# Kernel optimization log

Measured on AMD Instinct MI355X. Metric: run time of the kernel, lower is better.

## Reference

```python
import jax, jax.numpy as jnp
import numpy as np

B, C, HZ, SX = 512, 112, 8, 16
P = HZ * HZ   # num_kernel = 64 template pixels
OC = 256
EPS = 1e-5

def _conv(x, w, pad, groups=1):
    return jax.lax.conv_general_dilated(
        x, w, (1, 1), [(pad, pad), (pad, pad)],
        feature_group_count=groups,
        dimension_numbers=('NCHW', 'OIHW', 'NCHW'))

def _bn(x, g, b, m, v):
    # eval-mode BatchNorm2d with running stats
    scale = (g / jnp.sqrt(v + EPS))[None, :, None, None]
    return (x - m[None, :, None, None]) * scale + b[None, :, None, None]

def setup_inputs() -> dict:
    key = jax.random.key(0)
    ks = jax.random.split(key, 16)
    n = lambda i, shape, s=0.05: jax.random.normal(ks[i], shape, dtype=jnp.float32) * s
    return dict(
        search=jax.random.normal(ks[0], (B, C, SX, SX), dtype=jnp.float32),
        kernel=jax.random.normal(ks[1], (B, C, HZ, HZ), dtype=jnp.float32),
        ca_w1=n(2, (P, P)), ca_b1=jnp.zeros((P,), jnp.float32),
        ca_w2=n(3, (P, P)), ca_b2=jnp.zeros((P,), jnp.float32),
        cls_dw=n(4, (P, 1, 3, 3)), cls_pw=n(5, (OC, P)),
        cls_bn_g=jnp.ones((OC,), jnp.float32), cls_bn_b=jnp.zeros((OC,), jnp.float32),
        cls_bn_m=n(6, (OC,)), cls_bn_v=jax.random.uniform(ks[7], (OC,), jnp.float32, 0.5, 1.5),
        cls_pred_w=n(8, (1, OC, 3, 3)), cls_pred_b=jnp.zeros((1,), jnp.float32),
        box_dw=n(9, (P, 1, 3, 3)), box_pw=n(10, (OC, P)),
        box_bn_g=jnp.ones((OC,), jnp.float32), box_bn_b=jnp.zeros((OC,), jnp.float32),
        box_bn_m=n(11, (OC,)), box_bn_v=jax.random.uniform(ks[12], (OC,), jnp.float32, 0.5, 1.5),
        box_pred_w=n(13, (4, OC, 3, 3)), box_pred_b=jnp.zeros((4,), jnp.float32),
        adjust=0.1 * jnp.ones((1,), jnp.float32),
        bias_p=jnp.ones((1, 4, 1, 1), jnp.float32),
    )

def reference(search, kernel, ca_w1, ca_b1, ca_w2, ca_b2,
              cls_dw, cls_pw, cls_bn_g, cls_bn_b, cls_bn_m, cls_bn_v,
              cls_pred_w, cls_pred_b,
              box_dw, box_pw, box_bn_g, box_bn_b, box_bn_m, box_bn_v,
              box_pred_w, box_pred_b, adjust, bias_p):
    b, c, h, w = search.shape
    # pixel-wise correlation (batched form of the per-sample F.conv2d loop):
    # corr[b,p,i,j] = sum_c kernel[b,c].flatten()[p] * search[b,c,i,j]
    z = kernel.reshape(b, c, -1)                       # [B, C, P]
    corr = jnp.einsum('bcp,bcij->bpij', z, search)      # [B, P, H, W]
    # channel attention (CAModule, reduction=1)
    s = corr.mean(axis=(2, 3))                          # [B, P]
    a = jax.nn.sigmoid(jax.nn.relu(s @ ca_w1.T + ca_b1) @ ca_w2.T + ca_b2)
    corr = corr * a[:, :, None, None]
    # cls tower: depthwise 3x3 -> pointwise -> BN -> ReLU
    cfeat = jnp.einsum('oc,bchw->bohw', cls_pw, _conv(corr, cls_dw, 1, groups=P))
    cfeat = jax.nn.relu(_bn(cfeat, cls_bn_g, cls_bn_b, cls_bn_m, cls_bn_v))
    cls = 0.1 * (_conv(cfeat, cls_pred_w, 1) + cls_pred_b[None, :, None, None])
    # bbox tower
    rfeat = jnp.einsum('oc,bchw->bohw', box_pw, _conv(corr, box_dw, 1, groups=P))
    rfeat = jax.nn.relu(_bn(rfeat, box_bn_g, box_bn_b, box_bn_m, box_bn_v))
    pred = _conv(rfeat, box_pred_w, 1) + box_pred_b[None, :, None, None]
    x = jnp.exp(adjust[0] * pred + bias_p)
    return (x, cls)
```

## Files before the change

### kernel.cpp

```cpp
#include <hip/hip_runtime.h>
#include <hip/hip_bf16.h>


typedef __attribute__((ext_vector_type(8))) short  bf16x8;
typedef __attribute__((ext_vector_type(4))) float  f32x4;

union U8 { bf16x8 v; uint4 q; unsigned short u[8]; };

__device__ __forceinline__ float bf2f(unsigned short h){
  union { unsigned int u; float f; } c; c.u = ((unsigned int)h) << 16; return c.f;
}
__device__ __forceinline__ unsigned short f2bf(float f){
  return __bfloat16_as_ushort(__float2bfloat16(f));
}
__device__ __forceinline__ unsigned int f2bf2(float lo, float hi){
  return (unsigned int)f2bf(lo) | ((unsigned int)f2bf(hi) << 16);
}

__device__ __forceinline__ int swz(int row, int pix){
  return row*256 + (((pix>>3) ^ (row&31))<<3) + (pix&7);
}
__device__ __forceinline__ int zt_off(int p, int c){
  return (p<<8) + ((((c>>3) ^ (p&15)) & 15)<<4) + ((c&7)<<1);
}
__device__ __forceinline__ int sT_off(int pix, int c){
  return (pix<<7) + ((((c>>3) ^ (pix&7) ^ ((pix>>3)&7)) & 7)<<4) + ((c&7)<<1);
}
__device__ __forceinline__ int dT_off(int pix, int p){
  return (pix<<7) + (((((p>>3) ^ pix) & 7)) << 4) + ((p & 7) << 1);
}
__device__ __forceinline__ int fT_off(int pix, int ocl){
  return (pix<<6) + ((((ocl>>3) ^ pix ^ (pix>>2)) & 3) << 4) + ((ocl & 7) << 1);
}
__device__ __forceinline__ int pA_off(int ocl, int p){
  return (ocl<<7) + (((((p>>3) ^ ocl) & 7)) << 4) + ((p & 7) << 1);
}

__device__ __forceinline__ void stage_pw(int tid, int oc0,
                                         const float* __restrict__ pw,
                                         unsigned char* __restrict__ dst){
  const int ocl = tid >> 4, p0 = (tid & 15) << 2;
  const float4 f0 = *(const float4*)&pw[(oc0 + ocl)*64 + p0];
  uint2 w; w.x = f2bf2(f0.x, f0.y); w.y = f2bf2(f0.z, f0.w);
  *(uint2*)(dst + pA_off(ocl, p0)) = w;
}

template<int NOUT>
__device__ __forceinline__ void stage_wA(int tid, int oc0,
                                         const float* __restrict__ pdw,
                                         unsigned char* __restrict__ dst){
  #pragma unroll
  for (int i=0;i<(NOUT*288+511)/512;++i){
    const int idx = i*512 + tid;
    if (idx < NOUT*288){
      const int o   = idx / 288;
      const int rem = idx - o*288;
      const int tau = rem >> 5, ocl = rem & 31;
      *(unsigned short*)(dst + (idx<<1)) =
          f2bf(pdw[(o*256 + oc0 + ocl)*9 + tau]);
    }
  }
}

template<int NOUT, bool DBUF>
__device__ __forceinline__ void run_tower(
    int tid, float ap,
    const float* __restrict__ dw,  const float* __restrict__ pw,
    const float* __restrict__ bng, const float* __restrict__ bnb,
    const float* __restrict__ bnm, const float* __restrict__ bnv,
    const float* __restrict__ pdw, const float* __restrict__ pdb,
    float* __restrict__ outp, float adj, const float* __restrict__ biasp,
    unsigned char* smem)
{
  const int lane = tid & 63, wave = tid >> 6;
  const int l15 = lane & 15, lg = lane >> 4;
  unsigned short* sA16 = (unsigned short*)smem;

  {
    const int p = lane;
    unsigned char* dT = smem + 32768;
    float wd[9];
    #pragma unroll
    for (int k=0;k<9;++k) wd[k] = dw[p*9+k] * ap;
    #pragma unroll
    for (int io=0;io<2;++io){
      const int ir = wave*2 + io;
      float ot[16];
      #pragma unroll
      for (int j=0;j<16;++j) ot[j] = 0.f;
      #pragma unroll
      for (int dr=0;dr<3;++dr){
        const int r = ir-1+dr;
        if (r >= 0 && r < 16){
          unsigned short tr[16];
          *(uint4*)&tr[0] = *(uint4*)&sA16[swz(p, r*16)];
          *(uint4*)&tr[8] = *(uint4*)&sA16[swz(p, r*16 + 8)];
          float rr[16];
          #pragma unroll
          for (int j=0;j<16;++j) rr[j] = bf2f(tr[j]);
          const float w0 = wd[dr*3+0], w1 = wd[dr*3+1], w2 = wd[dr*3+2];
          #pragma unroll
          for (int j=0;j<16;++j){
            float s = w1*rr[j];
            if (j > 0)  s = fmaf(w0, rr[j-1], s);
            if (j < 15) s = fmaf(w2, rr[j+1], s);
            ot[j] += s;
          }
        }
      }
      #pragma unroll
      for (int j=0;j<16;++j)
        *(unsigned short*)(dT + dT_off(ir*16+j, p)) = f2bf(ot[j]);
    }
  }
  __syncthreads();

  U8 bfr[2][2];
  #pragma unroll
  for (int nt=0;nt<2;++nt)
    #pragma unroll
    for (int ks=0;ks<2;++ks)
      bfr[nt][ks].q = *(const uint4*)(smem + 32768 +
          dT_off(wave*32 + nt*16 + l15, ks*32 + lg*8));
  __syncthreads();

  float* scl = (float*)(smem + 61952);
  float* bia = (float*)(smem + 62976);
  if (tid < 256){
    const float s = bng[tid] * rsqrtf(bnv[tid] + 1e-5f);
    scl[tid] = s;
    bia[tid] = bnb[tid] - bnm[tid]*s;
  }

  f32x4 accp[2];
  accp[0] = f32x4{0.f,0.f,0.f,0.f};
  accp[1] = f32x4{0.f,0.f,0.f,0.f};

  auto pw_chunk = [&](unsigned char* pAb, unsigned char* featb, int oc0){
    #pragma unroll
    for (int mt=0;mt<2;++mt){
      U8 af0, af1;
      af0.q = *(const uint4*)(pAb + pA_off(mt*16 + l15, lg*8));
      af1.q = *(const uint4*)(pAb + pA_off(mt*16 + l15, 32 + lg*8));
      f32x4 accw[2];
      accw[0] = f32x4{0.f,0.f,0.f,0.f};
      accw[1] = f32x4{0.f,0.f,0.f,0.f};
      #pragma unroll
      for (int nt=0;nt<2;++nt){
        accw[nt] = __builtin_amdgcn_mfma_f32_16x16x32_bf16(
            af0.v, bfr[nt][0].v, accw[nt], 0, 0, 0);
        accw[nt] = __builtin_amdgcn_mfma_f32_16x16x32_bf16(
            af1.v, bfr[nt][1].v, accw[nt], 0, 0, 0);
      }
      #pragma unroll
      for (int r=0;r<4;++r){
        const int ocl = mt*16 + lg*4 + r;
        const float sc = scl[oc0+ocl], bi = bia[oc0+ocl];
        #pragma unroll
        for (int nt=0;nt<2;++nt){
          const int pix = wave*32 + nt*16 + l15;
          const float v = fmaxf(fmaf(accw[nt][r], sc, bi), 0.f);
          *(unsigned short*)(featb + fT_off(pix, ocl)) = f2bf(v);
        }
      }
    }
  };

  auto pred_chunk = [&](unsigned char* featb, unsigned char* wAb){
    #pragma unroll
    for (int dr=0;dr<3;++dr){
      #pragma unroll
      for (int dc=0;dc<3;++dc){
        const int tau = dr*3 + dc;
        U8 a;
        const int mr = (NOUT == 4) ? (l15 & 3) : 0;
        a.q = *(const uint4*)(wAb + ((mr*288 + tau*32 + lg*8) << 1));
        if (l15 >= NOUT) a.q = make_uint4(0u,0u,0u,0u);
        #pragma unroll
        for (int nt=0;nt<2;++nt){
          const int rp = wave*2 + nt + dr - 1;
          if (rp >= 0 && rp <= 15){
            const int cp = l15 + dc - 1;
            const int cc = cp < 0 ? 0 : (cp > 15 ? 15 : cp);
            U8 bf;
            bf.q = *(const uint4*)(featb + fT_off(rp*16 + cc, lg*8));
            if (cp != cc) bf.q = make_uint4(0u,0u,0u,0u);
            accp[nt] = __builtin_amdgcn_mfma_f32_16x16x32_bf16(
                a.v, bf.v, accp[nt], 0, 0, 0);
          }
        }
      }
    }
  };

  if constexpr (!DBUF){
    stage_pw(tid, 0, pw, smem + 49152);
    stage_wA<NOUT>(tid, 0, pdw, smem + 57344);
    for (int ch=0; ch<8; ++ch){
      const int buf = ch & 1, oc0 = ch*32;
      __syncthreads();
      pw_chunk(smem + 49152 + buf*4096, smem + 32768, oc0);
      __syncthreads();
      if (ch < 7){
        stage_pw(tid, oc0 + 32, pw, smem + 49152 + (buf^1)*4096);
        stage_wA<NOUT>(tid, oc0 + 32, pdw, smem + 57344 + (buf^1)*2304);
      }
      pred_chunk(smem + 32768, smem + 57344 + buf*2304);
    }
    __syncthreads();
  } else {
    stage_pw(tid, 0,  pw, smem + 49152);
    stage_pw(tid, 32, pw, smem + 53248);
    stage_wA<NOUT>(tid, 0, pdw, smem + 57344);
    __syncthreads();
    pw_chunk(smem + 49152, smem + 0, 0);
    __syncthreads();
    for (int i=0; i<8; ++i){
      const int s = i & 1;
      if (i < 6) stage_pw(tid, (i+2)*32, pw, smem + 49152 + s*4096);
      if (i < 7) stage_wA<NOUT>(tid, (i+1)*32, pdw,
                                smem + 57344 + ((i+1)&1)*(NOUT*576));
      if (i < 7) pw_chunk(smem + 49152 + ((i+1)&1)*4096,
                          smem + ((i+1)&1)*16384, (i+1)*32);
      pred_chunk(smem + s*16384, smem + 57344 + s*(NOUT*576));
      __syncthreads();
    }
  }

  if (lane < 16){
    #pragma unroll
    for (int nt=0;nt<2;++nt){
      const int rt = wave*2 + nt;
      if constexpr (NOUT == 1){
        outp[rt*16 + lane] = 0.1f*(accp[nt][0] + pdb[0]);
      } else {
        #pragma unroll
        for (int o=0;o<4;++o)
          outp[o*256 + rt*16 + lane] =
              expf(fmaf(adj, accp[nt][o] + pdb[o], biasp[o]));
      }
    }
  }
}

__global__ __launch_bounds__(512, 4) void fused_head(
  const float* __restrict__ search, const float* __restrict__ kern,
  const float* __restrict__ ca_w1, const float* __restrict__ ca_b1,
  const float* __restrict__ ca_w2, const float* __restrict__ ca_b2,
  const float* __restrict__ cls_dw, const float* __restrict__ cls_pw,
  const float* __restrict__ cls_bn_g, const float* __restrict__ cls_bn_b,
  const float* __restrict__ cls_bn_m, const float* __restrict__ cls_bn_v,
  const float* __restrict__ cls_pred_w, const float* __restrict__ cls_pred_b,
  const float* __restrict__ box_dw, const float* __restrict__ box_pw,
  const float* __restrict__ box_bn_g, const float* __restrict__ box_bn_b,
  const float* __restrict__ box_bn_m, const float* __restrict__ box_bn_v,
  const float* __restrict__ box_pred_w, const float* __restrict__ box_pred_b,
  const float* __restrict__ adjust, const float* __restrict__ bias_p,
  float* __restrict__ out)
{
  __shared__ __align__(16) unsigned char smem[65536];
  const int b   = blockIdx.x;
  const int tid = threadIdx.x;
  const int lane = tid & 63, wave = tid >> 6;
  const int l15 = lane & 15, lg = lane >> 4;

  unsigned char* zb = smem;
  {
    const float* kb = kern + (size_t)b*7168;
    #pragma unroll
    for (int i=0;i<14;++i){
      const int idx = i*512 + tid;
      const int c = idx>>6, p = idx&63;
      *(unsigned short*)(zb + zt_off(p,c)) = f2bf(kb[idx]);
    }
    #pragma unroll
    for (int i=0;i<2;++i){
      const int idx = i*512 + tid;
      const int p = idx>>4, c = 112 + (idx&15);
      *(unsigned short*)(zb + zt_off(p,c)) = 0;
    }
  }

  unsigned char* stb = smem + 16384;
  const float* sea = search + (size_t)b*28672;
  f32x4 acc[4][2];
  #pragma unroll
  for (int mt=0;mt<4;++mt)
    #pragma unroll
    for (int nt=0;nt<2;++nt) acc[mt][nt] = f32x4{0.f,0.f,0.f,0.f};

  for (int kc=0;kc<2;++kc){
    __syncthreads();
    #pragma unroll
    for (int i=0;i<8;++i){
      const int f4i = i*512 + tid;
      const int cc = f4i>>6, pix0 = (f4i&63)<<2;
      const int c  = kc*64 + cc;
      float4 v;
      if (c < 112) v = *(const float4*)(sea + c*256 + pix0);
      else         v = make_float4(0.f,0.f,0.f,0.f);
      const float vv[4] = {v.x, v.y, v.z, v.w};
      #pragma unroll
      for (int j=0;j<4;++j)
        *(unsigned short*)(stb + sT_off(pix0+j, cc)) = f2bf(vv[j]);
    }
    __syncthreads();
    #pragma unroll
    for (int kt=0;kt<2;++kt){
      U8 bh[2];
      #pragma unroll
      for (int nt=0;nt<2;++nt){
        const int pix = wave*32 + nt*16 + l15;
        bh[nt].q = *(const uint4*)(stb + sT_off(pix, kt*32 + lg*8));
      }
      #pragma unroll
      for (int mt=0;mt<4;++mt){
        U8 ah;
        ah.q = *(const uint4*)(zb + zt_off(mt*16 + l15, kc*64 + kt*32 + lg*8));
        #pragma unroll
        for (int nt=0;nt<2;++nt)
          acc[mt][nt] = __builtin_amdgcn_mfma_f32_16x16x32_bf16(
              ah.v, bh[nt].v, acc[mt][nt], 0, 0, 0);
      }
    }
  }
  __syncthreads();

  unsigned short* sA16 = (unsigned short*)smem;
  #pragma unroll
  for (int mt=0;mt<4;++mt){
    #pragma unroll
    for (int nt=0;nt<2;++nt){
      const int pix = wave*32 + nt*16 + l15;
      #pragma unroll
      for (int r=0;r<4;++r)
        sA16[swz(mt*16 + lg*4 + r, pix)] = f2bf(acc[mt][nt][r]);
    }
  }

  float* ws    = (float*)(smem + 49152);
  float* smean = (float*)(smem + 51200);
  float* h1    = (float*)(smem + 51456);
  float* attvG = (float*)(smem + 51712);
  #pragma unroll
  for (int mt=0;mt<4;++mt){
    #pragma unroll
    for (int r=0;r<4;++r){
      float s = acc[mt][0][r] + acc[mt][1][r];
      s += __shfl_xor(s, 1, 64);
      s += __shfl_xor(s, 2, 64);
      s += __shfl_xor(s, 4, 64);
      s += __shfl_xor(s, 8, 64);
      if (l15 == 0) ws[wave*64 + mt*16 + lg*4 + r] = s;
    }
  }
  __syncthreads();
  if (tid < 64){
    float m = 0.f;
    #pragma unroll
    for (int w=0;w<8;++w) m += ws[w*64 + tid];
    smean[tid] = m * (1.f/256.f);
  }
  __syncthreads();
  if (tid < 64){
    float s = ca_b1[tid];
    const float* wr = ca_w1 + tid*64;
    #pragma unroll 8
    for (int k=0;k<64;++k) s += smean[k]*wr[k];
    h1[tid] = fmaxf(s, 0.f);
  }
  __syncthreads();
  if (tid < 64){
    float s = ca_b2[tid];
    const float* wr = ca_w2 + tid*64;
    #pragma unroll 8
    for (int k=0;k<64;++k) s += h1[k]*wr[k];
    attvG[tid] = 1.f/(1.f + expf(-s));
  }
  __syncthreads();
  const float ap = attvG[lane];
  __syncthreads();

  const float adj = adjust[0];

  run_tower<1,false>(tid, ap, cls_dw, cls_pw, cls_bn_g, cls_bn_b, cls_bn_m,
                     cls_bn_v, cls_pred_w, cls_pred_b,
                     out + 524288 + (size_t)b*256, adj, bias_p, smem);
  run_tower<4,true >(tid, ap, box_dw, box_pw, box_bn_g, box_bn_b, box_bn_m,
                     box_bn_v, box_pred_w, box_pred_b,
                     out + (size_t)b*1024, adj, bias_p, smem);
}

extern "C" void kernel_launch(void* const* d_in, const int* in_sizes, int n_in,
                              void* d_out, int out_size, void* d_ws, size_t ws_size,
                              hipStream_t stream) {
  (void)in_sizes; (void)n_in; (void)d_ws; (void)ws_size; (void)out_size;
  const float* search     = (const float*)d_in[0];
  const float* kern       = (const float*)d_in[1];
  const float* ca_w1      = (const float*)d_in[2];
  const float* ca_b1      = (const float*)d_in[3];
  const float* ca_w2      = (const float*)d_in[4];
  const float* ca_b2      = (const float*)d_in[5];
  const float* cls_dw     = (const float*)d_in[6];
  const float* cls_pw     = (const float*)d_in[7];
  const float* cls_bn_g   = (const float*)d_in[8];
  const float* cls_bn_b   = (const float*)d_in[9];
  const float* cls_bn_m   = (const float*)d_in[10];
  const float* cls_bn_v   = (const float*)d_in[11];
  const float* cls_pred_w = (const float*)d_in[12];
  const float* cls_pred_b = (const float*)d_in[13];
  const float* box_dw     = (const float*)d_in[14];
  const float* box_pw     = (const float*)d_in[15];
  const float* box_bn_g   = (const float*)d_in[16];
  const float* box_bn_b   = (const float*)d_in[17];
  const float* box_bn_m   = (const float*)d_in[18];
  const float* box_bn_v   = (const float*)d_in[19];
  const float* box_pred_w = (const float*)d_in[20];
  const float* box_pred_b = (const float*)d_in[21];
  const float* adjust     = (const float*)d_in[22];
  const float* bias_p     = (const float*)d_in[23];

  hipLaunchKernelGGL(fused_head, dim3(512), dim3(512), 0, stream,
    search, kern, ca_w1, ca_b1, ca_w2, ca_b2,
    cls_dw, cls_pw, cls_bn_g, cls_bn_b, cls_bn_m, cls_bn_v,
    cls_pred_w, cls_pred_b,
    box_dw, box_pw, box_bn_g, box_bn_b, box_bn_m, box_bn_v,
    box_pred_w, box_pred_b, adjust, bias_p,
    (float*)d_out);
}
```

Measured before the change: 76.79 us.

## Interleave cls and box towers in one shared-barrier chunk loop

Replaces the two sequential tower passes with a single schedule. Both depthwise convolutions run back to back, each wave reads its own MFMA B fragments without a block barrier, and the pointwise and prediction work for both towers is interleaved over the same eight output-channel chunks. The goal is to cut the number of __syncthreads, merge weight staging and BN setup for both towers, and give the scheduler more independent MFMA work per barrier. In exchange it keeps two sets of fragments and accumulators live, which raises register pressure, and it drops the box tower's separate software-pipelined double-buffer path.

```diff
diff --git a/kernel.cpp b/kernel.cpp
--- a/kernel.cpp
+++ b/kernel.cpp
@@ -62,182 +62,107 @@
   }
 }
 
-template<int NOUT, bool DBUF>
-__device__ __forceinline__ void run_tower(
-    int tid, float ap,
-    const float* __restrict__ dw,  const float* __restrict__ pw,
-    const float* __restrict__ bng, const float* __restrict__ bnb,
-    const float* __restrict__ bnm, const float* __restrict__ bnv,
-    const float* __restrict__ pdw, const float* __restrict__ pdb,
-    float* __restrict__ outp, float adj, const float* __restrict__ biasp,
-    unsigned char* smem)
+__device__ __forceinline__ void dw_phase(
+    int lane, int wave, float ap, const float* __restrict__ dw,
+    const unsigned short* __restrict__ sA16, unsigned char* __restrict__ dT)
 {
-  const int lane = tid & 63, wave = tid >> 6;
-  const int l15 = lane & 15, lg = lane >> 4;
-  unsigned short* sA16 = (unsigned short*)smem;
-
-  {
-    const int p = lane;
-    unsigned char* dT = smem + 32768;
-    float wd[9];
-    #pragma unroll
-    for (int k=0;k<9;++k) wd[k] = dw[p*9+k] * ap;
-    #pragma unroll
-    for (int io=0;io<2;++io){
-      const int ir = wave*2 + io;
-      float ot[16];
-      #pragma unroll
-      for (int j=0;j<16;++j) ot[j] = 0.f;
-      #pragma unroll
-      for (int dr=0;dr<3;++dr){
-        const int r = ir-1+dr;
-        if (r >= 0 && r < 16){
-          unsigned short tr[16];
-          *(uint4*)&tr[0] = *(uint4*)&sA16[swz(p, r*16)];
-          *(uint4*)&tr[8] = *(uint4*)&sA16[swz(p, r*16 + 8)];
-          float rr[16];
-          #pragma unroll
-          for (int j=0;j<16;++j) rr[j] = bf2f(tr[j]);
-          const float w0 = wd[dr*3+0], w1 = wd[dr*3+1], w2 = wd[dr*3+2];
-          #pragma unroll
-          for (int j=0;j<16;++j){
-            float s = w1*rr[j];
-            if (j > 0)  s = fmaf(w0, rr[j-1], s);
-            if (j < 15) s = fmaf(w2, rr[j+1], s);
-            ot[j] += s;
-          }
+  const int p = lane;
+  float wd[9];
+  #pragma unroll
+  for (int k=0;k<9;++k) wd[k] = dw[p*9+k] * ap;
+  #pragma unroll
+  for (int io=0;io<2;++io){
+    const int ir = wave*2 + io;
+    float ot[16];
+    #pragma unroll
+    for (int j=0;j<16;++j) ot[j] = 0.f;
+    #pragma unroll
+    for (int dr=0;dr<3;++dr){
+      const int r = ir-1+dr;
+      if (r >= 0 && r < 16){
+        unsigned short tr[16];
+        *(uint4*)&tr[0] = *(uint4*)&sA16[swz(p, r*16)];
+        *(uint4*)&tr[8] = *(uint4*)&sA16[swz(p, r*16 + 8)];
+        float rr[16];
+        #pragma unroll
+        for (int j=0;j<16;++j) rr[j] = bf2f(tr[j]);
+        const float w0 = wd[dr*3+0], w1 = wd[dr*3+1], w2 = wd[dr*3+2];
+        #pragma unroll
+        for (int j=0;j<16;++j){
+          float s = w1*rr[j];
+          if (j > 0)  s = fmaf(w0, rr[j-1], s);
+          if (j < 15) s = fmaf(w2, rr[j+1], s);
+          ot[j] += s;
         }
       }
-      #pragma unroll
-      for (int j=0;j<16;++j)
-        *(unsigned short*)(dT + dT_off(ir*16+j, p)) = f2bf(ot[j]);
-    }
-  }
-  __syncthreads();
-
-  U8 bfr[2][2];
-  #pragma unroll
-  for (int nt=0;nt<2;++nt)
-    #pragma unroll
-    for (int ks=0;ks<2;++ks)
-      bfr[nt][ks].q = *(const uint4*)(smem + 32768 +
-          dT_off(wave*32 + nt*16 + l15, ks*32 + lg*8));
-  __syncthreads();
-
-  float* scl = (float*)(smem + 61952);
-  float* bia = (float*)(smem + 62976);
-  if (tid < 256){
-    const float s = bng[tid] * rsqrtf(bnv[tid] + 1e-5f);
-    scl[tid] = s;
-    bia[tid] = bnb[tid] - bnm[tid]*s;
-  }
-
-  f32x4 accp[2];
-  accp[0] = f32x4{0.f,0.f,0.f,0.f};
-  accp[1] = f32x4{0.f,0.f,0.f,0.f};
-
-  auto pw_chunk = [&](unsigned char* pAb, unsigned char* featb, int oc0){
-    #pragma unroll
-    for (int mt=0;mt<2;++mt){
-      U8 af0, af1;
-      af0.q = *(const uint4*)(pAb + pA_off(mt*16 + l15, lg*8));
-      af1.q = *(const uint4*)(pAb + pA_off(mt*16 + l15, 32 + lg*8));
-      f32x4 accw[2];
-      accw[0] = f32x4{0.f,0.f,0.f,0.f};
-      accw[1] = f32x4{0.f,0.f,0.f,0.f};
+    }
+    #pragma unroll
+    for (int j=0;j<16;++j)
+      *(unsigned short*)(dT + dT_off(ir*16+j, p)) = f2bf(ot[j]);
+  }
+}
+
+__device__ __forceinline__ void pw_phase(
+    int l15, int lg, int wave, const U8 bfr[2][2],
+    const unsigned char* __restrict__ pAb, unsigned char* __restrict__ featb,
+    const float* __restrict__ scl, const float* __restrict__ bia, int oc0)
+{
+  #pragma unroll
+  for (int mt=0;mt<2;++mt){
+    U8 af0, af1;
+    af0.q = *(const uint4*)(pAb + pA_off(mt*16 + l15, lg*8));
+    af1.q = *(const uint4*)(pAb + pA_off(mt*16 + l15, 32 + lg*8));
+    f32x4 accw[2];
+    accw[0] = f32x4{0.f,0.f,0.f,0.f};
+    accw[1] = f32x4{0.f,0.f,0.f,0.f};
+    #pragma unroll
+    for (int nt=0;nt<2;++nt){
+      accw[nt] = __builtin_amdgcn_mfma_f32_16x16x32_bf16(
+          af0.v, bfr[nt][0].v, accw[nt], 0, 0, 0);
+      accw[nt] = __builtin_amdgcn_mfma_f32_16x16x32_bf16(
+          af1.v, bfr[nt][1].v, accw[nt], 0, 0, 0);
+    }
+    #pragma unroll
+    for (int r=0;r<4;++r){
+      const int ocl = mt*16 + lg*4 + r;
+      const float sc = scl[oc0+ocl], bi = bia[oc0+ocl];
       #pragma unroll
       for (int nt=0;nt<2;++nt){
-        accw[nt] = __builtin_amdgcn_mfma_f32_16x16x32_bf16(
-            af0.v, bfr[nt][0].v, accw[nt], 0, 0, 0);
-        accw[nt] = __builtin_amdgcn_mfma_f32_16x16x32_bf16(
-            af1.v, bfr[nt][1].v, accw[nt], 0, 0, 0);
+        const int pix = wave*32 + nt*16 + l15;
+        const float v = fmaxf(fmaf(accw[nt][r], sc, bi), 0.f);
+        *(unsigned short*)(featb + fT_off(pix, ocl)) = f2bf(v);
       }
-      #pragma unroll
-      for (int r=0;r<4;++r){
-        const int ocl = mt*16 + lg*4 + r;
-        const float sc = scl[oc0+ocl], bi = bia[oc0+ocl];
-        #pragma unroll
-        for (int nt=0;nt<2;++nt){
-          const int pix = wave*32 + nt*16 + l15;
-          const float v = fmaxf(fmaf(accw[nt][r], sc, bi), 0.f);
-          *(unsigned short*)(featb + fT_off(pix, ocl)) = f2bf(v);
+    }
+  }
+}
+
+template<int NOUT>
+__device__ __forceinline__ void pred_phase(
+    int l15, int lg, int wave,
+    const unsigned char* __restrict__ featb,
+    const unsigned char* __restrict__ wAb, f32x4* accp)
+{
+  #pragma unroll
+  for (int dr=0;dr<3;++dr){
+    #pragma unroll
+    for (int dc=0;dc<3;++dc){
+      const int tau = dr*3 + dc;
+      U8 a;
+      const int mr = (NOUT == 4) ? (l15 & 3) : 0;
+      a.q = *(const uint4*)(wAb + ((mr*288 + tau*32 + lg*8) << 1));
+      if (l15 >= NOUT) a.q = make_uint4(0u,0u,0u,0u);
+      #pragma unroll
+      for (int nt=0;nt<2;++nt){
+        const int rp = wave*2 + nt + dr - 1;
+        if (rp >= 0 && rp <= 15){
+          const int cp = l15 + dc - 1;
+          const int cc = cp < 0 ? 0 : (cp > 15 ? 15 : cp);
+          U8 bf;
+          bf.q = *(const uint4*)(featb + fT_off(rp*16 + cc, lg*8));
+          if (cp != cc) bf.q = make_uint4(0u,0u,0u,0u);
+          accp[nt] = __builtin_amdgcn_mfma_f32_16x16x32_bf16(
+              a.v, bf.v, accp[nt], 0, 0, 0);
         }
-      }
-    }
-  };
-
-  auto pred_chunk = [&](unsigned char* featb, unsigned char* wAb){
-    #pragma unroll
-    for (int dr=0;dr<3;++dr){
-      #pragma unroll
-      for (int dc=0;dc<3;++dc){
-        const int tau = dr*3 + dc;
-        U8 a;
-        const int mr = (NOUT == 4) ? (l15 & 3) : 0;
-        a.q = *(const uint4*)(wAb + ((mr*288 + tau*32 + lg*8) << 1));
-        if (l15 >= NOUT) a.q = make_uint4(0u,0u,0u,0u);
-        #pragma unroll
-        for (int nt=0;nt<2;++nt){
-          const int rp = wave*2 + nt + dr - 1;
-          if (rp >= 0 && rp <= 15){
-            const int cp = l15 + dc - 1;
-            const int cc = cp < 0 ? 0 : (cp > 15 ? 15 : cp);
-            U8 bf;
-            bf.q = *(const uint4*)(featb + fT_off(rp*16 + cc, lg*8));
-            if (cp != cc) bf.q = make_uint4(0u,0u,0u,0u);
-            accp[nt] = __builtin_amdgcn_mfma_f32_16x16x32_bf16(
-                a.v, bf.v, accp[nt], 0, 0, 0);
-          }
-        }
-      }
-    }
-  };
-
-  if constexpr (!DBUF){
-    stage_pw(tid, 0, pw, smem + 49152);
-    stage_wA<NOUT>(tid, 0, pdw, smem + 57344);
-    for (int ch=0; ch<8; ++ch){
-      const int buf = ch & 1, oc0 = ch*32;
-      __syncthreads();
-      pw_chunk(smem + 49152 + buf*4096, smem + 32768, oc0);
-      __syncthreads();
-      if (ch < 7){
-        stage_pw(tid, oc0 + 32, pw, smem + 49152 + (buf^1)*4096);
-        stage_wA<NOUT>(tid, oc0 + 32, pdw, smem + 57344 + (buf^1)*2304);
-      }
-      pred_chunk(smem + 32768, smem + 57344 + buf*2304);
-    }
-    __syncthreads();
-  } else {
-    stage_pw(tid, 0,  pw, smem + 49152);
-    stage_pw(tid, 32, pw, smem + 53248);
-    stage_wA<NOUT>(tid, 0, pdw, smem + 57344);
-    __syncthreads();
-    pw_chunk(smem + 49152, smem + 0, 0);
-    __syncthreads();
-    for (int i=0; i<8; ++i){
-      const int s = i & 1;
-      if (i < 6) stage_pw(tid, (i+2)*32, pw, smem + 49152 + s*4096);
-      if (i < 7) stage_wA<NOUT>(tid, (i+1)*32, pdw,
-                                smem + 57344 + ((i+1)&1)*(NOUT*576));
-      if (i < 7) pw_chunk(smem + 49152 + ((i+1)&1)*4096,
-                          smem + ((i+1)&1)*16384, (i+1)*32);
-      pred_chunk(smem + s*16384, smem + 57344 + s*(NOUT*576));
-      __syncthreads();
-    }
-  }
-
-  if (lane < 16){
-    #pragma unroll
-    for (int nt=0;nt<2;++nt){
-      const int rt = wave*2 + nt;
-      if constexpr (NOUT == 1){
-        outp[rt*16 + lane] = 0.1f*(accp[nt][0] + pdb[0]);
-      } else {
-        #pragma unroll
-        for (int o=0;o<4;++o)
-          outp[o*256 + rt*16 + lane] =
-              expf(fmaf(adj, accp[nt][o] + pdb[o], biasp[o]));
       }
     }
   }
@@ -383,12 +308,75 @@
 
   const float adj = adjust[0];
 
-  run_tower<1,false>(tid, ap, cls_dw, cls_pw, cls_bn_g, cls_bn_b, cls_bn_m,
-                     cls_bn_v, cls_pred_w, cls_pred_b,
-                     out + 524288 + (size_t)b*256, adj, bias_p, smem);
-  run_tower<4,true >(tid, ap, box_dw, box_pw, box_bn_g, box_bn_b, box_bn_m,
-                     box_bn_v, box_pred_w, box_pred_b,
-                     out + (size_t)b*1024, adj, bias_p, smem);
+  unsigned char* dT = smem + 32768;
+  U8 bfr_cls[2][2], bfr_box[2][2];
+  dw_phase(lane, wave, ap, cls_dw, sA16, dT);
+  #pragma unroll
+  for (int nt=0;nt<2;++nt)
+    #pragma unroll
+    for (int ks=0;ks<2;++ks)
+      bfr_cls[nt][ks].q = *(const uint4*)(dT +
+          dT_off(wave*32 + nt*16 + l15, ks*32 + lg*8));
+  dw_phase(lane, wave, ap, box_dw, sA16, dT);
+  #pragma unroll
+  for (int nt=0;nt<2;++nt)
+    #pragma unroll
+    for (int ks=0;ks<2;++ks)
+      bfr_box[nt][ks].q = *(const uint4*)(dT +
+          dT_off(wave*32 + nt*16 + l15, ks*32 + lg*8));
+  __syncthreads();
+
+  float* sclc = (float*)(smem + 54912);
+  float* biac = (float*)(smem + 55936);
+  float* sclb = (float*)(smem + 56960);
+  float* biab = (float*)(smem + 57984);
+  if (tid < 256){
+    float s = cls_bn_g[tid] * rsqrtf(cls_bn_v[tid] + 1e-5f);
+    sclc[tid] = s; biac[tid] = cls_bn_b[tid] - cls_bn_m[tid]*s;
+    s = box_bn_g[tid] * rsqrtf(box_bn_v[tid] + 1e-5f);
+    sclb[tid] = s; biab[tid] = box_bn_b[tid] - box_bn_m[tid]*s;
+  }
+  stage_pw(tid, 0, cls_pw, smem + 32768);
+  stage_pw(tid, 0, box_pw, smem + 40960);
+  stage_wA<1>(tid, 0, cls_pred_w, smem + 49152);
+  stage_wA<4>(tid, 0, box_pred_w, smem + 50304);
+
+  f32x4 apc[2], apb[2];
+  apc[0] = f32x4{0.f,0.f,0.f,0.f}; apc[1] = f32x4{0.f,0.f,0.f,0.f};
+  apb[0] = f32x4{0.f,0.f,0.f,0.f}; apb[1] = f32x4{0.f,0.f,0.f,0.f};
+
+  for (int ch=0; ch<8; ++ch){
+    const int buf = ch & 1, oc0 = ch*32;
+    __syncthreads();
+
+    pw_phase(l15, lg, wave, bfr_cls, smem + 32768 + buf*4096,
+             smem + 0,     sclc, biac, oc0);
+    pw_phase(l15, lg, wave, bfr_box, smem + 40960 + buf*4096,
+             smem + 16384, sclb, biab, oc0);
+    __syncthreads();
+
+    if (ch < 7){
+      stage_pw(tid, oc0 + 32, cls_pw, smem + 32768 + (buf^1)*4096);
+      stage_pw(tid, oc0 + 32, box_pw, smem + 40960 + (buf^1)*4096);
+      stage_wA<1>(tid, oc0 + 32, cls_pred_w, smem + 49152 + (buf^1)*576);
+      stage_wA<4>(tid, oc0 + 32, box_pred_w, smem + 50304 + (buf^1)*2304);
+    }
+    pred_phase<1>(l15, lg, wave, smem + 0,     smem + 49152 + buf*576,  apc);
+    pred_phase<4>(l15, lg, wave, smem + 16384, smem + 50304 + buf*2304, apb);
+  }
+
+  if (lane < 16){
+    #pragma unroll
+    for (int nt=0;nt<2;++nt){
+      const int rt = wave*2 + nt;
+      out[524288 + (size_t)b*256 + rt*16 + lane] =
+          0.1f*(apc[nt][0] + cls_pred_b[0]);
+      #pragma unroll
+      for (int o=0;o<4;++o)
+        out[(size_t)b*1024 + o*256 + rt*16 + lane] =
+            expf(fmaf(adj, apb[nt][o] + box_pred_b[o], bias_p[o]));
+    }
+  }
 }
 
 extern "C" void kernel_launch(void* const* d_in, const int* in_sizes, int n_in,
```

Result: slower. 84.18 us (+9.6%).
